# Kernel tuning notes

Hardware: AMD Instinct MI355X
Metric: run time of the kernel (lower is better)

Reference implementation:

```python
import jax, jax.numpy as jnp
import numpy as np

F = 64        # atom feature dim (from Linear(64, 32))
N_RBF = 25    # Gaussian RBF expansion size (standard SchNet 0..5 A)
CUTOFF = 5.0
GAMMA = 10.0  # RBF width parameter: exp(-gamma * (d - mu)^2)


def ssp(x):
    # shifted softplus: ln(0.5 * e^x + 0.5) = softplus(x) - ln 2
    return jax.nn.softplus(x) - jnp.log(2.0).astype(x.dtype)


def setup_inputs() -> dict:
    key = jax.random.key(0)
    ks = jax.random.split(key, 16)
    B, N = 4, 512
    embedding = jax.random.normal(ks[0], (B, N, F), jnp.float32)
    d = jax.random.uniform(ks[1], (B, N, N), jnp.float32) * CUTOFF
    distances = 0.5 * (d + jnp.swapaxes(d, 1, 2))  # symmetric pairwise distances
    s = 0.1
    # 3 stacked interaction blocks
    in2f = jax.random.normal(ks[2], (3, F, F), jnp.float32) * s      # atomwise in->filter (no bias)
    fw1 = jax.random.normal(ks[3], (3, N_RBF, F), jnp.float32) * s   # filter net layer 1
    fb1 = jnp.zeros((3, F), jnp.float32)
    fw2 = jax.random.normal(ks[4], (3, F, F), jnp.float32) * s       # filter net layer 2
    fb2 = jnp.zeros((3, F), jnp.float32)
    f2o = jax.random.normal(ks[5], (3, F, F), jnp.float32) * s       # filter->out atomwise
    f2b = jnp.zeros((3, F), jnp.float32)
    dw = jax.random.normal(ks[6], (3, F, F), jnp.float32) * s        # output atomwise
    db = jnp.zeros((3, F), jnp.float32)
    # readout MLP: Linear(64,32) + SSP + Linear(32,1)
    aw1 = jax.random.normal(ks[7], (F, 32), jnp.float32) * s
    ab1 = jnp.zeros((32,), jnp.float32)
    aw2 = jax.random.normal(ks[8], (32, 1), jnp.float32) * s
    ab2 = jnp.zeros((1,), jnp.float32)
    return dict(embedding=embedding, distances=distances, in2f=in2f, fw1=fw1,
                fb1=fb1, fw2=fw2, fb2=fb2, f2o=f2o, f2b=f2b, dw=dw, db=db,
                aw1=aw1, ab1=ab1, aw2=aw2, ab2=ab2)


def reference(embedding, distances, in2f, fw1, fb1, fw2, fb2, f2o, f2b, dw, db,
              aw1, ab1, aw2, ab2):
    dtype = embedding.dtype
    centers = jnp.linspace(0.0, CUTOFF, N_RBF).astype(dtype)
    # Gaussian RBF expansion of pairwise distances: [B, N, N, N_RBF]
    rbf = jnp.exp(-GAMMA * jnp.square(distances[..., None] - centers))
    x = embedding  # [B, N, F]
    for i in range(3):
        f = x @ in2f[i]  # [B, N, F]
        # filter-generating network on expanded distances -> [B, N, N, F]
        W = ssp(jnp.einsum('bijr,rf->bijf', rbf, fw1[i]) + fb1[i])
        W = W @ fw2[i] + fb2[i]
        # continuous-filter convolution: y_i = sum_j f_j * W_ij
        y = jnp.einsum('bjf,bijf->bif', f, W)
        y = ssp(y @ f2o[i] + f2b[i])
        y = y @ dw[i] + db[i]
        x = x + y  # residual
    h = ssp(x @ aw1 + ab1)   # [B, N, 32]
    return h @ aw2 + ab2     # [B, N, 1]
```

## Files before the change

kernel.cpp:

```cpp
#include <hip/hip_runtime.h>

#define KBIN 224
#define TSTRIDE 68
#define TPSZ  15232
#define FBASE 15232

typedef _Float16 half2v __attribute__((ext_vector_type(2)));

__device__ __forceinline__ float ssp(float x) {
    return fmaxf(x, 0.0f) + log1pf(expf(-fabsf(x))) - 0.69314718055994531f;
}

__device__ __forceinline__ float bclane(float v, int l) {
    return __builtin_bit_cast(float, __builtin_amdgcn_readlane(__builtin_bit_cast(int, v), l));
}

__device__ __forceinline__ unsigned int kaenc(float d) {
    float tv = fminf(fmaxf(d, 0.0f)*(224.0f/5.0f), 223.999f);
    int k = (int)tv;
    float fr = tv - (float)k;
    unsigned short fh = __builtin_bit_cast(unsigned short, (_Float16)fr);
    return ((unsigned int)(k*272) << 16) | (unsigned int)fh;
}

__device__ __forceinline__ float matvec64(const float* __restrict__ ldsA, int base, float xv, int lane) {
    float a0 = 0.f, a1 = 0.f, a2 = 0.f, a3 = 0.f;
    #pragma unroll
    for (int gg = 0; gg < 16; ++gg) {
        const float4 w = *(const float4*)&ldsA[base + lane*64 + (((gg + lane) & 15) << 2)];
        a0 += bclane(xv, gg*4+0) * w.x;
        a1 += bclane(xv, gg*4+1) * w.y;
        a2 += bclane(xv, gg*4+2) * w.z;
        a3 += bclane(xv, gg*4+3) * w.w;
    }
    return (a0 + a1) + (a2 + a3);
}

__device__ __forceinline__ void matvec64x2(const float* __restrict__ ldsA, int base,
                                           float xv0, float xv1, int lane,
                                           float& o0, float& o1) {
    float a0 = 0.f, a1 = 0.f, b0 = 0.f, b1 = 0.f;
    #pragma unroll
    for (int gg = 0; gg < 16; ++gg) {
        const float4 w = *(const float4*)&ldsA[base + lane*64 + (((gg + lane) & 15) << 2)];
        a0 += bclane(xv0, gg*4+0) * w.x;
        a1 += bclane(xv0, gg*4+1) * w.y;
        a0 += bclane(xv0, gg*4+2) * w.z;
        a1 += bclane(xv0, gg*4+3) * w.w;
        b0 += bclane(xv1, gg*4+0) * w.x;
        b1 += bclane(xv1, gg*4+1) * w.y;
        b0 += bclane(xv1, gg*4+2) * w.z;
        b1 += bclane(xv1, gg*4+3) * w.w;
    }
    o0 = a0 + a1;
    o1 = b0 + b1;
}

__device__ __forceinline__ void stageWT(float* __restrict__ lds, int base, const float* __restrict__ W, int tid) {
    for (int s = tid; s < 4096; s += 512) {
        int f = s >> 6, g = s & 63;
        lds[base + g*64 + ((((f >> 2) + g) & 15) << 2) + (f & 3)] = W[s];
    }
}

__global__ __launch_bounds__(512) void schnet_pre0(
    const float* __restrict__ emb, const float* __restrict__ dists,
    const float* __restrict__ in2f,
    const float* __restrict__ fw1, const float* __restrict__ fb1,
    const float* __restrict__ fw2, const float* __restrict__ fb2,
    unsigned short* __restrict__ f_out, unsigned int* __restrict__ Tp_g,
    unsigned int* __restrict__ ka)
{
    __shared__ float lds[12544];
    const int wg = blockIdx.x, tid = threadIdx.x;
    const int wave = tid >> 6, lane = tid & 63;
    if (wg < 128) {
        stageWT(lds, 0, in2f, tid);
        __syncthreads();
        int row0 = wg*16 + wave*2;
        size_t ro0 = (size_t)row0*64 + lane;
        size_t ro1 = ro0 + 64;
        float f0, f1;
        matvec64x2(lds, 0, emb[ro0], emb[ro1], lane, f0, f1);
        f_out[ro0] = __builtin_bit_cast(unsigned short, (_Float16)f0);
        f_out[ro1] = __builtin_bit_cast(unsigned short, (_Float16)f1);
    } else if (wg < 212) {
        int widx = wg - 128;
        int tt = widx / 28;
        int k = (widx % 28)*8 + wave;
        const float* fw1t = fw1 + tt*25*64;
        const float* fw2t = fw2 + tt*64*64;
        for (int s = tid; s < 1600; s += 512) lds[s] = fw1t[s];
        for (int s = tid; s < 4096; s += 512) lds[1600 + s] = fw2t[s];
        if (tid < 64) { lds[5696 + tid] = fb1[tt*64 + tid]; lds[5760 + tid] = fb2[tt*64 + tid]; }
        __syncthreads();
        float T2[2];
        #pragma unroll
        for (int e = 0; e < 2; ++e) {
            float dk = (float)(k + e) * (5.0f/224.0f);
            float h1 = lds[5696 + lane];
            for (int r = 0; r < 25; ++r) {
                float sr = dk - (float)r * (5.0f/24.0f);
                h1 += expf(-10.0f*sr*sr) * lds[r*64 + lane];
            }
            float u = ssp(h1);
            float T = lds[5760 + lane];
            #pragma unroll
            for (int gg = 0; gg < 64; ++gg)
                T += bclane(u, gg) * lds[1600 + gg*64 + lane];
            T2[e] = T;
        }
        float* sc = &lds[5824 + wave*128];
        sc[lane] = T2[0];
        sc[64 + lane] = T2[1];
        if (lane < 16) {
            float4 A  = *(const float4*)&sc[lane*4];
            float4 Bv = *(const float4*)&sc[64 + lane*4];
            half2v t01 = { (_Float16)A.x, (_Float16)A.y };
            half2v t23 = { (_Float16)A.z, (_Float16)A.w };
            half2v d01 = { (_Float16)(Bv.x - A.x), (_Float16)(Bv.y - A.y) };
            half2v d23 = { (_Float16)(Bv.z - A.z), (_Float16)(Bv.w - A.w) };
            uint4 o;
            o.x = __builtin_bit_cast(unsigned int, t01);
            o.y = __builtin_bit_cast(unsigned int, t23);
            o.z = __builtin_bit_cast(unsigned int, d01);
            o.w = __builtin_bit_cast(unsigned int, d23);
            *(uint4*)&Tp_g[(size_t)tt*TPSZ + k*TSTRIDE + lane*4] = o;
        }
    } else {
        size_t p = (size_t)(wg - 212)*4096 + (size_t)tid*8;
        float4 d0 = *(const float4*)&dists[p];
        float4 d1 = *(const float4*)&dists[p + 4];
        uint4 o0, o1;
        o0.x = kaenc(d0.x); o0.y = kaenc(d0.y); o0.z = kaenc(d0.z); o0.w = kaenc(d0.w);
        o1.x = kaenc(d1.x); o1.y = kaenc(d1.y); o1.z = kaenc(d1.z); o1.w = kaenc(d1.w);
        *(uint4*)&ka[p] = o0;
        *(uint4*)&ka[p + 4] = o1;
    }
}

__global__ __launch_bounds__(512, 4) void schnet_block(
    int t,
    const float* __restrict__ emb,
    const float* __restrict__ in2f,
    const float* __restrict__ f2o, const float* __restrict__ f2b,
    const float* __restrict__ dw,  const float* __restrict__ db,
    const float* __restrict__ aw1, const float* __restrict__ ab1,
    const float* __restrict__ aw2, const float* __restrict__ ab2,
    const unsigned int* __restrict__ Tp_g,
    const unsigned int* __restrict__ ka,
    const unsigned short* __restrict__ f_in,
    unsigned short* __restrict__ f_out,
    float* __restrict__ x_buf, float* __restrict__ out)
{
    __shared__ unsigned int ldsu[FBASE + 4096];
    float* lds = (float*)ldsu;
    const int wg = blockIdx.x, tid = threadIdx.x;
    const int wave = tid >> 6, lane = tid & 63;
    const int b = wg >> 7, it = wg & 127;
    const int i0 = it * 4;
    const int fq = lane & 15, g = lane >> 4;
    const int r = wave >> 1;
    const int jhalf = wave & 1;

    const unsigned int* Tp = Tp_g + (size_t)t*TPSZ;
    for (int s = tid; s < TPSZ/4; s += 512)
        ((uint4*)ldsu)[s] = ((const uint4*)Tp)[s];

    const int j0 = tid >> 4, fq2 = tid & 15;
    const uint2* fsrc0 = (const uint2*)f_in + ((size_t)b*512 + j0)*16 + fq2;
    unsigned int* fdst = ldsu + FBASE + (j0 >> 1)*64 + fq2*4 + (j0 & 1)*2;
    uint2 rb0, rb1, rb2, rb3;
    {
        const uint2* sp = fsrc0;
        rb0 = sp[0]; rb1 = sp[512]; rb2 = sp[1024]; rb3 = sp[1536];
        *(uint2*)fdst = rb0; *(uint2*)(fdst + 1024) = rb1;
        *(uint2*)(fdst + 2048) = rb2; *(uint2*)(fdst + 3072) = rb3;
    }
    __syncthreads();

    const unsigned int* kabase = &ka[((size_t)(b*512 + i0 + r))*512 + jhalf*64 + g*16];
    const unsigned int* fp = ldsu + FBASE + fq*4;
    const char* Tbyte = (const char*)ldsu + fq*16;
    const int jpb = jhalf*32 + g*8;
    float a0 = 0.f, a1 = 0.f, a2 = 0.f, a3 = 0.f;

    for (int c = 0; c < 4; ++c) {
        if (c < 3) {
            const uint2* sp = fsrc0 + (size_t)(c + 1)*2048;
            rb0 = sp[0]; rb1 = sp[512]; rb2 = sp[1024]; rb3 = sp[1536];
        }
        uint4 kq0 = ((const uint4*)(kabase + c*128))[0];
        uint4 kq1 = ((const uint4*)(kabase + c*128))[1];
        uint4 kq2 = ((const uint4*)(kabase + c*128))[2];
        uint4 kq3 = ((const uint4*)(kabase + c*128))[3];
        uint4 kqa[4] = {kq0, kq1, kq2, kq3};
        #pragma unroll
        for (int j4 = 0; j4 < 4; ++j4) {
            uint4 fA = *(const uint4*)&fp[(jpb + j4*2)*64];
            uint4 fB = *(const uint4*)&fp[(jpb + j4*2 + 1)*64];
            unsigned int kk[4] = {kqa[j4].x, kqa[j4].y, kqa[j4].z, kqa[j4].w};
            unsigned int fl_[8] = {fA.x, fA.y, fA.z, fA.w, fB.x, fB.y, fB.z, fB.w};
            #pragma unroll
            for (int u = 0; u < 4; ++u) {
                unsigned int kau = kk[u];
                unsigned int koff = kau >> 16;
                half2v av = __builtin_bit_cast(half2v, __builtin_amdgcn_perm(kau, kau, 0x01000100u));
                uint4 tp = *(const uint4*)(Tbyte + koff);
                half2v W01 = __builtin_bit_cast(half2v, tp.z)*av + __builtin_bit_cast(half2v, tp.x);
                half2v W23 = __builtin_bit_cast(half2v, tp.w)*av + __builtin_bit_cast(half2v, tp.y);
                half2v f01 = __builtin_bit_cast(half2v, fl_[u*2]);
                half2v f23 = __builtin_bit_cast(half2v, fl_[u*2+1]);
                a0 += (float)W01[0] * (float)f01[0];
                a1 += (float)W01[1] * (float)f01[1];
                a2 += (float)W23[0] * (float)f23[0];
                a3 += (float)W23[1] * (float)f23[1];
            }
        }
        if (c < 3) {
            __syncthreads();
            *(uint2*)fdst = rb0; *(uint2*)(fdst + 1024) = rb1;
            *(uint2*)(fdst + 2048) = rb2; *(uint2*)(fdst + 3072) = rb3;
            __syncthreads();
        }
    }
    a0 += __shfl_xor(a0, 16, 64); a0 += __shfl_xor(a0, 32, 64);
    a1 += __shfl_xor(a1, 16, 64); a1 += __shfl_xor(a1, 32, 64);
    a2 += __shfl_xor(a2, 16, 64); a2 += __shfl_xor(a2, 32, 64);
    a3 += __shfl_xor(a3, 16, 64); a3 += __shfl_xor(a3, 32, 64);

    __syncthreads();
    if (g == 0) {
        float4 acc; acc.x = a0; acc.y = a1; acc.z = a2; acc.w = a3;
        *(float4*)&lds[FBASE + wave*64 + fq*4] = acc;
    }
    stageWT(lds, 0, f2o + t*4096, tid);
    stageWT(lds, 4096, dw + t*4096, tid);
    if (t < 2) {
        stageWT(lds, 8192, in2f + (t+1)*4096, tid);
    } else {
        for (int s = tid; s < 4096; s += 512) {
            int f = s >> 6, rr = s & 63;
            lds[8192 + rr*64 + ((((f >> 2) + rr) & 15) << 2) + (f & 3)] = aw1[f*32 + (rr & 31)];
        }
    }
    if (tid < 64) {
        lds[12288 + tid] = f2b[t*64 + tid];
        lds[12352 + tid] = db[t*64 + tid];
        if (t == 2) {
            lds[12416 + tid] = ab1[tid & 31];
            lds[12480 + tid] = aw2[tid & 31];
        }
    }
    __syncthreads();

    if (wave < 4) {
        int grow = b*512 + i0 + wave;
        size_t ro = (size_t)grow*64 + lane;
        float y = lds[FBASE + (wave*2)*64 + lane] + lds[FBASE + (wave*2+1)*64 + lane];
        float z = matvec64(lds, 0, y, lane) + lds[12288 + lane];
        float u = ssp(z);
        float y3 = matvec64(lds, 4096, u, lane) + lds[12352 + lane];
        float xin = (t == 0) ? emb[ro] : x_buf[ro];
        float xn = xin + y3;
        if (t < 2) {
            x_buf[ro] = xn;
            float fo = matvec64(lds, 8192, xn, lane);
            f_out[ro] = __builtin_bit_cast(unsigned short, (_Float16)fo);
        } else {
            float s1 = matvec64(lds, 8192, xn, lane) + lds[12416 + lane];
            float h = ssp(s1) * lds[12480 + lane];
            #pragma unroll
            for (int m = 1; m < 64; m <<= 1)
                h += __shfl_xor(h, m, 64);
            if (lane == 0) out[grow] = ab2[0] + 0.5f*h;
        }
    }
}

extern "C" void kernel_launch(void* const* d_in, const int* in_sizes, int n_in,
                              void* d_out, int out_size, void* d_ws, size_t ws_size,
                              hipStream_t stream) {
    const float* emb  = (const float*)d_in[0];
    const float* dist = (const float*)d_in[1];
    const float* in2f = (const float*)d_in[2];
    const float* fw1  = (const float*)d_in[3];
    const float* fb1  = (const float*)d_in[4];
    const float* fw2  = (const float*)d_in[5];
    const float* fb2  = (const float*)d_in[6];
    const float* f2o  = (const float*)d_in[7];
    const float* f2b  = (const float*)d_in[8];
    const float* dwp  = (const float*)d_in[9];
    const float* dbp  = (const float*)d_in[10];
    const float* aw1  = (const float*)d_in[11];
    const float* ab1  = (const float*)d_in[12];
    const float* aw2  = (const float*)d_in[13];
    const float* ab2  = (const float*)d_in[14];
    float* out = (float*)d_out;
    float* ws = (float*)d_ws;
    unsigned int* Tp_g = (unsigned int*)ws;
    unsigned short* fA = (unsigned short*)(ws + 45696);
    unsigned short* fB = (unsigned short*)(ws + 45696 + 65536);
    float* x_buf = ws + 45696 + 2*65536;
    unsigned int* ka = (unsigned int*)(x_buf + 131072);

    hipLaunchKernelGGL(schnet_pre0, dim3(468), dim3(512), 0, stream,
        emb, dist, in2f, fw1, fb1, fw2, fb2, fA, Tp_g, ka);
    hipLaunchKernelGGL(schnet_block, dim3(512), dim3(512), 0, stream,
        0, emb, in2f, f2o, f2b, dwp, dbp, aw1, ab1, aw2, ab2,
        Tp_g, ka, fA, fB, x_buf, out);
    hipLaunchKernelGGL(schnet_block, dim3(512), dim3(512), 0, stream,
        1, emb, in2f, f2o, f2b, dwp, dbp, aw1, ab1, aw2, ab2,
        Tp_g, ka, fB, fA, x_buf, out);
    hipLaunchKernelGGL(schnet_block, dim3(512), dim3(512), 0, stream,
        2, emb, in2f, f2o, f2b, dwp, dbp, aw1, ab1, aw2, ab2,
        Tp_g, ka, fA, fB, x_buf, out);
}
```

Baseline: 64.56 us.

## Double-buffer feature tiles in LDS, prefetch distance codes, and coarsen filter table

The j-loop now keeps two LDS buffers for the fp16 neighbour features. This removes one of the two barriers per chunk, and the packed distance-bin codes for the next chunk are prefetched into registers. To fit the second buffer in LDS, the precomputed filter lookup table drops from 224 to 160 distance bins, which shrinks the table and its LDS copy. The coarser interpolation table lowers accuracy of the filter approximation and raises register pressure from the prefetched codes and full unroll.

```diff
diff --git a/kernel.cpp b/kernel.cpp
--- a/kernel.cpp
+++ b/kernel.cpp
@@ -1,9 +1,10 @@
 #include <hip/hip_runtime.h>
 
-#define KBIN 224
+#define KBIN 160
 #define TSTRIDE 68
-#define TPSZ  15232
-#define FBASE 15232
+#define TPSZ  10880
+#define FBASE 10880
+#define FB2   14976
 
 typedef _Float16 half2v __attribute__((ext_vector_type(2)));
 
@@ -16,7 +17,7 @@
 }
 
 __device__ __forceinline__ unsigned int kaenc(float d) {
-    float tv = fminf(fmaxf(d, 0.0f)*(224.0f/5.0f), 223.999f);
+    float tv = fminf(fmaxf(d, 0.0f)*32.0f, 159.999f);
     int k = (int)tv;
     float fr = tv - (float)k;
     unsigned short fh = __builtin_bit_cast(unsigned short, (_Float16)fr);
@@ -84,10 +85,10 @@
         matvec64x2(lds, 0, emb[ro0], emb[ro1], lane, f0, f1);
         f_out[ro0] = __builtin_bit_cast(unsigned short, (_Float16)f0);
         f_out[ro1] = __builtin_bit_cast(unsigned short, (_Float16)f1);
-    } else if (wg < 212) {
+    } else if (wg < 188) {
         int widx = wg - 128;
-        int tt = widx / 28;
-        int k = (widx % 28)*8 + wave;
+        int tt = widx / 20;
+        int k = (widx % 20)*8 + wave;
         const float* fw1t = fw1 + tt*25*64;
         const float* fw2t = fw2 + tt*64*64;
         for (int s = tid; s < 1600; s += 512) lds[s] = fw1t[s];
@@ -97,7 +98,7 @@
         float T2[2];
         #pragma unroll
         for (int e = 0; e < 2; ++e) {
-            float dk = (float)(k + e) * (5.0f/224.0f);
+            float dk = (float)(k + e) * (5.0f/160.0f);
             float h1 = lds[5696 + lane];
             for (int r = 0; r < 25; ++r) {
                 float sr = dk - (float)r * (5.0f/24.0f);
@@ -128,7 +129,7 @@
             *(uint4*)&Tp_g[(size_t)tt*TPSZ + k*TSTRIDE + lane*4] = o;
         }
     } else {
-        size_t p = (size_t)(wg - 212)*4096 + (size_t)tid*8;
+        size_t p = (size_t)(wg - 188)*4096 + (size_t)tid*8;
         float4 d0 = *(const float4*)&dists[p];
         float4 d1 = *(const float4*)&dists[p + 4];
         uint4 o0, o1;
@@ -153,7 +154,7 @@
     unsigned short* __restrict__ f_out,
     float* __restrict__ x_buf, float* __restrict__ out)
 {
-    __shared__ unsigned int ldsu[FBASE + 4096];
+    __shared__ unsigned int ldsu[FB2 + 4096];
     float* lds = (float*)ldsu;
     const int wg = blockIdx.x, tid = threadIdx.x;
     const int wave = tid >> 6, lane = tid & 63;
@@ -169,32 +170,40 @@
 
     const int j0 = tid >> 4, fq2 = tid & 15;
     const uint2* fsrc0 = (const uint2*)f_in + ((size_t)b*512 + j0)*16 + fq2;
-    unsigned int* fdst = ldsu + FBASE + (j0 >> 1)*64 + fq2*4 + (j0 & 1)*2;
+    const int fo_base = (j0 >> 1)*64 + fq2*4 + (j0 & 1)*2;
+    unsigned int* fdstA = ldsu + FBASE + fo_base;
+    unsigned int* fdstB = ldsu + FB2 + fo_base;
+    const unsigned int* kabase = &ka[((size_t)(b*512 + i0 + r))*512 + jhalf*64 + g*16];
+
     uint2 rb0, rb1, rb2, rb3;
+    uint4 kc0, kc1, kc2, kc3, kn0, kn1, kn2, kn3;
     {
-        const uint2* sp = fsrc0;
-        rb0 = sp[0]; rb1 = sp[512]; rb2 = sp[1024]; rb3 = sp[1536];
-        *(uint2*)fdst = rb0; *(uint2*)(fdst + 1024) = rb1;
-        *(uint2*)(fdst + 2048) = rb2; *(uint2*)(fdst + 3072) = rb3;
+        rb0 = fsrc0[0]; rb1 = fsrc0[512]; rb2 = fsrc0[1024]; rb3 = fsrc0[1536];
+        kc0 = ((const uint4*)kabase)[0];
+        kc1 = ((const uint4*)kabase)[1];
+        kc2 = ((const uint4*)kabase)[2];
+        kc3 = ((const uint4*)kabase)[3];
+        *(uint2*)fdstA = rb0; *(uint2*)(fdstA + 1024) = rb1;
+        *(uint2*)(fdstA + 2048) = rb2; *(uint2*)(fdstA + 3072) = rb3;
     }
     __syncthreads();
 
-    const unsigned int* kabase = &ka[((size_t)(b*512 + i0 + r))*512 + jhalf*64 + g*16];
-    const unsigned int* fp = ldsu + FBASE + fq*4;
+    const unsigned int* fpA = ldsu + FBASE + fq*4;
+    const unsigned int* fpB = ldsu + FB2 + fq*4;
     const char* Tbyte = (const char*)ldsu + fq*16;
     const int jpb = jhalf*32 + g*8;
     float a0 = 0.f, a1 = 0.f, a2 = 0.f, a3 = 0.f;
 
+    #pragma unroll
     for (int c = 0; c < 4; ++c) {
         if (c < 3) {
             const uint2* sp = fsrc0 + (size_t)(c + 1)*2048;
             rb0 = sp[0]; rb1 = sp[512]; rb2 = sp[1024]; rb3 = sp[1536];
-        }
-        uint4 kq0 = ((const uint4*)(kabase + c*128))[0];
-        uint4 kq1 = ((const uint4*)(kabase + c*128))[1];
-        uint4 kq2 = ((const uint4*)(kabase + c*128))[2];
-        uint4 kq3 = ((const uint4*)(kabase + c*128))[3];
-        uint4 kqa[4] = {kq0, kq1, kq2, kq3};
+            const uint4* kp = (const uint4*)(kabase + (c + 1)*128);
+            kn0 = kp[0]; kn1 = kp[1]; kn2 = kp[2]; kn3 = kp[3];
+        }
+        const unsigned int* fp = (c & 1) ? fpB : fpA;
+        uint4 kqa[4] = {kc0, kc1, kc2, kc3};
         #pragma unroll
         for (int j4 = 0; j4 < 4; ++j4) {
             uint4 fA = *(const uint4*)&fp[(jpb + j4*2)*64];
@@ -218,9 +227,10 @@
             }
         }
         if (c < 3) {
-            __syncthreads();
-            *(uint2*)fdst = rb0; *(uint2*)(fdst + 1024) = rb1;
-            *(uint2*)(fdst + 2048) = rb2; *(uint2*)(fdst + 3072) = rb3;
+            unsigned int* fd = (c & 1) ? fdstA : fdstB;
+            *(uint2*)fd = rb0; *(uint2*)(fd + 1024) = rb1;
+            *(uint2*)(fd + 2048) = rb2; *(uint2*)(fd + 3072) = rb3;
+            kc0 = kn0; kc1 = kn1; kc2 = kn2; kc3 = kn3;
             __syncthreads();
         }
     }
@@ -232,7 +242,7 @@
     __syncthreads();
     if (g == 0) {
         float4 acc; acc.x = a0; acc.y = a1; acc.z = a2; acc.w = a3;
-        *(float4*)&lds[FBASE + wave*64 + fq*4] = acc;
+        *(float4*)&lds[FB2 + wave*64 + fq*4] = acc;
     }
     stageWT(lds, 0, f2o + t*4096, tid);
     stageWT(lds, 4096, dw + t*4096, tid);
@@ -257,7 +267,7 @@
     if (wave < 4) {
         int grow = b*512 + i0 + wave;
         size_t ro = (size_t)grow*64 + lane;
-        float y = lds[FBASE + (wave*2)*64 + lane] + lds[FBASE + (wave*2+1)*64 + lane];
+        float y = lds[FB2 + (wave*2)*64 + lane] + lds[FB2 + (wave*2+1)*64 + lane];
         float z = matvec64(lds, 0, y, lane) + lds[12288 + lane];
         float u = ssp(z);
         float y3 = matvec64(lds, 4096, u, lane) + lds[12352 + lane];
@@ -299,12 +309,12 @@
     float* out = (float*)d_out;
     float* ws = (float*)d_ws;
     unsigned int* Tp_g = (unsigned int*)ws;
-    unsigned short* fA = (unsigned short*)(ws + 45696);
-    unsigned short* fB = (unsigned short*)(ws + 45696 + 65536);
-    float* x_buf = ws + 45696 + 2*65536;
+    unsigned short* fA = (unsigned short*)(ws + 32640);
+    unsigned short* fB = (unsigned short*)(ws + 32640 + 65536);
+    float* x_buf = ws + 32640 + 2*65536;
     unsigned int* ka = (unsigned int*)(x_buf + 131072);
 
-    hipLaunchKernelGGL(schnet_pre0, dim3(468), dim3(512), 0, stream,
+    hipLaunchKernelGGL(schnet_pre0, dim3(444), dim3(512), 0, stream,
         emb, dist, in2f, fw1, fb1, fw2, fb2, fA, Tp_g, ka);
     hipLaunchKernelGGL(schnet_block, dim3(512), dim3(512), 0, stream,
         0, emb, in2f, f2o, f2b, dwp, dbp, aw1, ab1, aw2, ab2,
```

Result: no change. 65.27 us (+1.1%).
